# Kernel optimization log

Measured on AMD Instinct MI355X. Metric: run time of the kernel, lower is better.

The kernel has to match this reference:

```python
import jax, jax.numpy as jnp
import numpy as np

B, S, HQ, HKV, D = 2, 2048, 32, 8, 128
ROPE_BASE = 10000.0
NEG_INF = -1e9


def setup_inputs() -> dict:
    key = jax.random.key(0)
    kq, kk, kv = jax.random.split(key, 3)
    q = jax.random.normal(kq, (B, S, HQ, D), dtype=jnp.float32)
    k = jax.random.normal(kk, (B, S, HKV, D), dtype=jnp.float32)
    v = jax.random.normal(kv, (B, S, HKV, D), dtype=jnp.float32)
    # Llama rotary tables: [S, D] with freqs duplicated across the two halves
    inv_freq = 1.0 / (ROPE_BASE ** (jnp.arange(0, D, 2, dtype=jnp.float32) / D))
    freqs = jnp.arange(S, dtype=jnp.float32)[:, None] * inv_freq[None, :]  # [S, D/2]
    emb = jnp.concatenate([freqs, freqs], axis=-1)  # [S, D]
    cos = jnp.cos(emb)
    sin = jnp.sin(emb)
    # causal additive mask [B, 1, S, S]: 0 on/below diagonal, -1e9 above
    causal = jnp.tril(jnp.ones((S, S), dtype=bool))
    attention_mask = jnp.where(causal, 0.0, NEG_INF).astype(jnp.float32)
    attention_mask = jnp.broadcast_to(attention_mask[None, None], (B, 1, S, S))
    return {
        "query_states": q,
        "key_states": k,
        "value_states": v,
        "cos": cos,
        "sin": sin,
        "attention_mask": attention_mask,
        "softmax_scale": float(1.0 / np.sqrt(D)),
    }


def _rotate_half(x):
    h = x.shape[-1] // 2
    return jnp.concatenate([-x[..., h:], x[..., :h]], axis=-1)


def _apply_rope(x, cos, sin):
    # x: [B, S, H, D]; cos/sin: [S, D] -> broadcast over batch and heads
    c = cos[None, :, None, :]
    s = sin[None, :, None, :]
    return x * c + _rotate_half(x) * s


def reference(query_states, key_states, value_states, cos, sin, attention_mask, softmax_scale):
    if attention_mask.ndim == 4 and attention_mask.shape[1] == 1:
        attention_mask = attention_mask[:, 0]  # [B, S, S]
    q = _apply_rope(query_states, cos, sin)          # [B, S, HQ, D]
    k = _apply_rope(key_states, cos, sin)            # [B, S, HKV, D]
    v = value_states                                  # [B, S, HKV, D]
    groups = q.shape[2] // k.shape[2]
    k = jnp.repeat(k, groups, axis=2)                 # [B, S, HQ, D]
    v = jnp.repeat(v, groups, axis=2)
    scores = jnp.einsum("bqhd,bkhd->bhqk", q, k) * softmax_scale
    scores = scores + attention_mask[:, None, :, :]   # broadcast over heads
    probs = jax.nn.softmax(scores, axis=-1)
    out = jnp.einsum("bhqk,bkhd->bqhd", probs, v)     # [B, S, HQ, D]
    return out
```

## Files before the change

kernel.cpp:

```cpp
#include <hip/hip_runtime.h>
#include <stdint.h>

typedef unsigned short u16;
typedef unsigned int   u32;
typedef short bf16x8 __attribute__((ext_vector_type(8)));
typedef u16   u16x8  __attribute__((ext_vector_type(8)));
typedef u16   u16x4  __attribute__((ext_vector_type(4)));
typedef float f32x4  __attribute__((ext_vector_type(4)));

#define B_   2
#define S_   2048
#define HQ_  32
#define HKV_ 8
#define D_   128
#define SC2  0.1275174457530659f

#define KR_ELEMS (B_*HKV_*S_*D_)

#define KT_BLOCKS ((B_*S_*HKV_*16) / 256)
#define VT_BLOCKS (B_*HKV_*(S_/64))

#define SWZ(x) ((x) ^ (((x) >> 3) & 0x70))

__device__ __forceinline__ float b2f(u16 x) { return __uint_as_float(((u32)x) << 16); }
__device__ __forceinline__ u16 f2b(float f) {
  u32 u = __float_as_uint(f);
  return (u16)((u + 0x7FFFu + ((u >> 16) & 1u)) >> 16);
}
__device__ __forceinline__ bool is_f32(const void* cs) {
  return ((const u32*)cs)[0] == 0x3F800000u;
}

#if __has_builtin(__builtin_amdgcn_exp2f)
#define EXP2(x) __builtin_amdgcn_exp2f(x)
#else
#define EXP2(x) exp2f(x)
#endif

__device__ __forceinline__ void pl32(u32& a, u32& b) {
  auto r = __builtin_amdgcn_permlane32_swap((int)a, (int)b, false, false);
  a = (u32)r[0]; b = (u32)r[1];
}
__device__ __forceinline__ void pl16(u32& a, u32& b) {
  auto r = __builtin_amdgcn_permlane16_swap((int)a, (int)b, false, false);
  a = (u32)r[0]; b = (u32)r[1];
}
__device__ __forceinline__ float qredmax(float x) {
  u32 a = __float_as_uint(x), b = a;
  pl16(a, b);
  float m = fmaxf(__uint_as_float(a), __uint_as_float(b));
  u32 c = __float_as_uint(m), d = c;
  pl32(c, d);
  return fmaxf(__uint_as_float(c), __uint_as_float(d));
}
__device__ __forceinline__ float qredsum(float x) {
  u32 a = __float_as_uint(x), b = a;
  pl16(a, b);
  float m = __uint_as_float(a) + __uint_as_float(b);
  u32 c = __float_as_uint(m), d = c;
  pl32(c, d);
  return __uint_as_float(c) + __uint_as_float(d);
}
__device__ __forceinline__ u32 cvtpk(float lo, float hi) {
  u32 r;
  asm("v_cvt_pk_bf16_f32 %0, %1, %2" : "=v"(r) : "v"(lo), "v"(hi));
  return r;
}

__device__ __forceinline__ void gload16(const u16* g, u16* l) {
  __builtin_amdgcn_global_load_lds(
      (const __attribute__((address_space(1))) u32*)g,
      (__attribute__((address_space(3))) u32*)l, 16, 0, 0);
}

__global__ __launch_bounds__(256) void rope_pre(
    const void* __restrict__ kin, const void* __restrict__ vin,
    const void* __restrict__ cs, const void* __restrict__ sn, u16* __restrict__ ws)
{
  const bool f32 = is_f32(cs);
  const int bx = blockIdx.x;
  const int t  = threadIdx.x;
  __shared__ u16 tile[64 * 136];

  if (bx < KT_BLOCKS) {
    int tid = bx*256 + t;
    int j4 = tid & 15;
    int s  = (tid >> 4) & (S_ - 1);
    int h  = (tid >> 15) & (HKV_ - 1);
    int b  = tid >> 18;
    int gi = ((b*S_ + s)*HKV_ + h)*D_ + 4*j4;
    int ci = s*D_ + 4*j4;
    float xa[4], xb[4], c[4], si[4];
    if (f32) {
      const float* kf = (const float*)kin;
      f32x4 a0 = *(const f32x4*)(kf + gi);
      f32x4 b0 = *(const f32x4*)(kf + gi + 64);
      f32x4 c0 = *(const f32x4*)((const float*)cs + ci);
      f32x4 s0 = *(const f32x4*)((const float*)sn + ci);
#pragma unroll
      for (int e = 0; e < 4; ++e) { xa[e]=a0[e]; xb[e]=b0[e]; c[e]=c0[e]; si[e]=s0[e]; }
    } else {
      const u16* kb16 = (const u16*)kin;
      u16x4 a0 = *(const u16x4*)(kb16 + gi);
      u16x4 b0 = *(const u16x4*)(kb16 + gi + 64);
      u16x4 c0 = *(const u16x4*)((const u16*)cs + ci);
      u16x4 s0 = *(const u16x4*)((const u16*)sn + ci);
#pragma unroll
      for (int e = 0; e < 4; ++e) { xa[e]=b2f(a0[e]); xb[e]=b2f(b0[e]); c[e]=b2f(c0[e]); si[e]=b2f(s0[e]); }
    }
    u16 o0[4], o1[4];
#pragma unroll
    for (int e = 0; e < 4; ++e) {
      o0[e] = f2b(xa[e]*c[e] - xb[e]*si[e]);
      o1[e] = f2b(xb[e]*c[e] + xa[e]*si[e]);
    }
    int oi = ((b*HKV_ + h)*S_ + s)*D_ + 4*j4;
    *(u16x4*)(ws + oi)      = *(u16x4*)o0;
    *(u16x4*)(ws + oi + 64) = *(u16x4*)o1;
  } else {
    int vb = bx - KT_BLOCKS;
    int sb = vb & 31;
    int h  = (vb >> 5) & (HKV_ - 1);
    int b  = vb >> 8;
    int s0 = sb * 64;
#pragma unroll
    for (int it = 0; it < 8; ++it) {
      int task = it*256 + t;
      int c4 = task & 31;
      int r  = task >> 5;
      int gi = ((b*S_ + s0 + r)*HKV_ + h)*D_ + 4*c4;
      u16 e[4];
      if (f32) {
        f32x4 a = *(const f32x4*)((const float*)vin + gi);
#pragma unroll
        for (int j = 0; j < 4; ++j) e[j] = f2b(a[j]);
      } else {
        u16x4 a = *(const u16x4*)((const u16*)vin + gi);
#pragma unroll
        for (int j = 0; j < 4; ++j) e[j] = a[j];
      }
      *(u16x4*)&tile[r*136 + 4*c4] = *(u16x4*)e;
    }
    __syncthreads();
    u32* vtd = (u32*)(ws + KR_ELEMS) + (b*HKV_ + h)*D_*(S_/2);
#pragma unroll
    for (int it = 0; it < 16; ++it) {
      int task = it*256 + t;
      int sp = task & 31, d = task >> 5;
      u32 lo = tile[(2*sp)*136 + d];
      u32 hi = tile[(2*sp + 1)*136 + d];
      vtd[d*(S_/2) + s0/2 + sp] = lo | (hi << 16);
    }
  }
}

__global__ __launch_bounds__(256, 3) void flash_attn(
    const void* __restrict__ qg, const void* __restrict__ cs, const void* __restrict__ sn,
    const u16* __restrict__ ws, float* __restrict__ out)
{
  __shared__ __attribute__((aligned(16))) u16 lds[16384];
  char* ldsc = (char*)lds;

  const bool f32 = is_f32(cs);
  const int t = threadIdx.x;
  const int lane = t & 63, w = t >> 6;
  const int lq = lane & 15, quad = lane >> 4;

  const int kq = (lq*64 + quad*16) ^ (((lq >> 1) & 7) << 4);

  int bx = blockIdx.x;
  int g = bx & 7, ii = bx >> 3;
  int combo = g*2 + (ii >> 6);
  int b = combo >> 3, kvh = combo & 7;
  int rr = ii & 63;
  int h   = kvh*4 + (rr & 3);
  int qt  = 15 - (rr >> 2);
  int q0  = qt * 128;
  const int nkb  = 4*qt + 4;
  const int diag = 4*qt + w;

  const u16* Kr = ws + (b*HKV_ + kvh)*S_*D_;
  const u16* Vt = ws + KR_ELEMS + (b*HKV_ + kvh)*D_*S_;

  const int aK0 = t*16, aK1 = t*16 + 4096;
  const int lA0 = SWZ(aK0), lA1 = SWZ(aK1);
  const u16* kg0 = Kr + ((lA0 >> 6) & 31)*D_ + (lA0 >> 11)*32 + ((lA0 >> 4) & 3)*8;
  const u16* kg1 = Kr + ((lA1 >> 6) & 31)*D_ + (lA1 >> 11)*32 + ((lA1 >> 4) & 3)*8;
  const u16* vg0 = Vt + (lA0 >> 6)*S_ + ((lA0 >> 4) & 3)*8;
  const u16* vg1 = Vt + (lA1 >> 6)*S_ + ((lA1 >> 4) & 3)*8;

#define STAGE(bufbyte, n0v) do {                                   \
    gload16(kg0 + (n0v)*D_, (u16*)(ldsc + (bufbyte) + aK0));       \
    gload16(kg1 + (n0v)*D_, (u16*)(ldsc + (bufbyte) + aK1));       \
    gload16(vg0 + (n0v),    (u16*)(ldsc + (bufbyte) + 8192 + aK0));\
    gload16(vg1 + (n0v),    (u16*)(ldsc + (bufbyte) + 8192 + aK1));\
  } while (0)

#pragma unroll
  for (int it = 0; it < 4; ++it) {
    int tp = it*256 + t;
    int row = tp >> 3, j = tp & 7;
    int qbase = ((b*S_ + q0 + row)*HQ_ + h)*D_ + 8*j;
    int cbase = (q0 + row)*D_ + 8*j;
    float a[8], bb[8], cc[8], ssv[8];
    if (f32) {
      const float* qf32 = (const float*)qg;
      f32x4 a0 = *(const f32x4*)(qf32 + qbase);
      f32x4 a1 = *(const f32x4*)(qf32 + qbase + 4);
      f32x4 b0 = *(const f32x4*)(qf32 + qbase + 64);
      f32x4 b1 = *(const f32x4*)(qf32 + qbase + 68);
      f32x4 c0 = *(const f32x4*)((const float*)cs + cbase);
      f32x4 c1 = *(const f32x4*)((const float*)cs + cbase + 4);
      f32x4 s0 = *(const f32x4*)((const float*)sn + cbase);
      f32x4 s1 = *(const f32x4*)((const float*)sn + cbase + 4);
#pragma unroll
      for (int e = 0; e < 4; ++e) {
        a[e] = a0[e];  a[4+e] = a1[e];  bb[e] = b0[e]; bb[4+e] = b1[e];
        cc[e] = c0[e]; cc[4+e] = c1[e]; ssv[e] = s0[e]; ssv[4+e] = s1[e];
      }
    } else {
      const u16* qb16 = (const u16*)qg;
      u16x8 xa = *(const u16x8*)(qb16 + qbase);
      u16x8 xb = *(const u16x8*)(qb16 + qbase + 64);
      u16x8 cv = *(const u16x8*)((const u16*)cs + cbase);
      u16x8 sv = *(const u16x8*)((const u16*)sn + cbase);
#pragma unroll
      for (int e = 0; e < 8; ++e) {
        a[e] = b2f(xa[e]); bb[e] = b2f(xb[e]);
        cc[e] = b2f(cv[e]); ssv[e] = b2f(sv[e]);
      }
    }
    u16 o0[8], o1[8];
#pragma unroll
    for (int e = 0; e < 8; ++e) {
      float C2 = cc[e]*SC2, S2 = ssv[e]*SC2;
      o0[e] = f2b(a[e]*C2 - bb[e]*S2);
      o1[e] = f2b(bb[e]*C2 + a[e]*S2);
    }
    int A0 = (j >> 2)*8192 + row*64 + (j & 3)*16;
    int A1 = A0 + 16384;
    *(u16x8*)(ldsc + SWZ(A0)) = *(u16x8*)o0;
    *(u16x8*)(ldsc + SWZ(A1)) = *(u16x8*)o1;
  }
  __syncthreads();
  bf16x8 qfA[4], qfB[4];
#pragma unroll
  for (int c = 0; c < 4; ++c) {
    qfA[c] = *(const bf16x8*)(ldsc + c*8192 + w*2048 + kq);
    qfB[c] = *(const bf16x8*)(ldsc + c*8192 + w*2048 + 1024 + kq);
  }
  asm volatile("s_waitcnt lgkmcnt(0)" ::: "memory");
  __syncthreads();

  f32x4 oA[8], oB[8];
#pragma unroll
  for (int dt = 0; dt < 8; ++dt) { oA[dt] = (f32x4){0,0,0,0}; oB[dt] = (f32x4){0,0,0,0}; }
  float mA = -1e30f, lA = 0.f, mB = -1e30f, lB = 0.f;
  const int qrowA = q0 + 32*w + lq;

  STAGE(0, 0);

  for (int kb = 0; kb < nkb; ++kb) {
    const int cur = kb & 1;
    asm volatile("" ::: "memory");
    __builtin_amdgcn_s_barrier();
    asm volatile("" ::: "memory");
    if (kb + 1 < nkb) {
      STAGE((cur ^ 1) << 14, (kb + 1)*32);
      asm volatile("s_waitcnt vmcnt(4)" ::: "memory");
    } else {
      asm volatile("s_waitcnt vmcnt(0)" ::: "memory");
    }
    __builtin_amdgcn_s_barrier();
    asm volatile("" ::: "memory");

    if (kb > diag) continue;

    const char* tb = ldsc + (cur << 14) + kq;

    f32x4 sA0 = {0,0,0,0}, sA1 = {0,0,0,0}, sB0 = {0,0,0,0}, sB1 = {0,0,0,0};
#pragma unroll
    for (int c = 0; c < 4; ++c) {
      bf16x8 k0 = *(const bf16x8*)(tb + c*2048);
      bf16x8 k1 = *(const bf16x8*)(tb + c*2048 + 1024);
      sA0 = __builtin_amdgcn_mfma_f32_16x16x32_bf16(k0, qfA[c], sA0, 0, 0, 0);
      sA1 = __builtin_amdgcn_mfma_f32_16x16x32_bf16(k1, qfA[c], sA1, 0, 0, 0);
      sB0 = __builtin_amdgcn_mfma_f32_16x16x32_bf16(k0, qfB[c], sB0, 0, 0, 0);
      sB1 = __builtin_amdgcn_mfma_f32_16x16x32_bf16(k1, qfB[c], sB1, 0, 0, 0);
    }

    float a0[4], a1[4], b0[4], b1[4];
#pragma unroll
    for (int r = 0; r < 4; ++r) { a0[r]=sA0[r]; a1[r]=sA1[r]; b0[r]=sB0[r]; b1[r]=sB1[r]; }
    if (kb == diag) {
#pragma unroll
      for (int r = 0; r < 4; ++r) {
        bool over = (quad*4 + r > lq);
        if (over) a0[r] = -1e30f;
        a1[r] = -1e30f;
        if (over) b1[r] = -1e30f;
      }
    }

    float mxA = fmaxf(fmaxf(fmaxf(a0[0],a0[1]), fmaxf(a0[2],a0[3])),
                      fmaxf(fmaxf(a1[0],a1[1]), fmaxf(a1[2],a1[3])));
    float mxB = fmaxf(fmaxf(fmaxf(b0[0],b0[1]), fmaxf(b0[2],b0[3])),
                      fmaxf(fmaxf(b1[0],b1[1]), fmaxf(b1[2],b1[3])));
    mxA = qredmax(mxA);
    mxB = qredmax(mxB);
    if (!__all((mxA - mA <= 11.5f) && (mxB - mB <= 11.5f))) {
      float mnA = fmaxf(mA, mxA), alA = EXP2(mA - mnA);
      float mnB = fmaxf(mB, mxB), alB = EXP2(mB - mnB);
      lA *= alA; lB *= alB;
#pragma unroll
      for (int dt = 0; dt < 8; ++dt) {
#pragma unroll
        for (int r = 0; r < 4; ++r) { oA[dt][r] *= alA; oB[dt][r] *= alB; }
      }
      mA = mnA; mB = mnB;
    }
    float pA0[4], pA1[4], pB0[4], pB1[4];
    float rsA = 0.f, rsB = 0.f;
#pragma unroll
    for (int r = 0; r < 4; ++r) {
      pA0[r] = EXP2(a0[r] - mA); pA1[r] = EXP2(a1[r] - mA);
      pB0[r] = EXP2(b0[r] - mB); pB1[r] = EXP2(b1[r] - mB);
      rsA += pA0[r] + pA1[r];    rsB += pB0[r] + pB1[r];
    }
    lA += qredsum(rsA);
    lB += qredsum(rsB);

    u32 YA0 = cvtpk(pA0[0], pA0[1]), YA1 = cvtpk(pA0[2], pA0[3]);
    u32 ZA0 = cvtpk(pA1[0], pA1[1]), ZA1 = cvtpk(pA1[2], pA1[3]);
    pl32(YA0, ZA0); pl16(YA0, ZA0);
    pl32(YA1, ZA1); pl16(YA1, ZA1);
    u32 YB0 = cvtpk(pB0[0], pB0[1]), YB1 = cvtpk(pB0[2], pB0[3]);
    u32 ZB0 = cvtpk(pB1[0], pB1[1]), ZB1 = cvtpk(pB1[2], pB1[3]);
    pl32(YB0, ZB0); pl16(YB0, ZB0);
    pl32(YB1, ZB1); pl16(YB1, ZB1);
    union { u32 wd[4]; bf16x8 v; } puA, puB;
    puA.wd[0] = YA0; puA.wd[1] = YA1; puA.wd[2] = ZA0; puA.wd[3] = ZA1;
    puB.wd[0] = YB0; puB.wd[1] = YB1; puB.wd[2] = ZB0; puB.wd[3] = ZB1;
    bf16x8 pfA = puA.v, pfB = puB.v;

#pragma unroll
    for (int dt = 0; dt < 8; ++dt) {
      bf16x8 vf = *(const bf16x8*)(tb + 8192 + dt*1024);
      oA[dt] = __builtin_amdgcn_mfma_f32_16x16x32_bf16(vf, pfA, oA[dt], 0, 0, 0);
      oB[dt] = __builtin_amdgcn_mfma_f32_16x16x32_bf16(vf, pfB, oB[dt], 0, 0, 0);
    }
  }

  float invA = 1.0f / lA, invB = 1.0f / lB;
  float* opA = out + ((b*S_ + qrowA)*HQ_ + h)*D_ + quad*4;
  float* opB = opA + 16*HQ_*D_;
#pragma unroll
  for (int dt = 0; dt < 8; ++dt) {
    f32x4 va = { oA[dt][0]*invA, oA[dt][1]*invA, oA[dt][2]*invA, oA[dt][3]*invA };
    f32x4 vb = { oB[dt][0]*invB, oB[dt][1]*invB, oB[dt][2]*invB, oB[dt][3]*invB };
    *(f32x4*)(opA + dt*16) = va;
    *(f32x4*)(opB + dt*16) = vb;
  }
#undef STAGE
}

extern "C" void kernel_launch(void* const* d_in, const int* in_sizes, int n_in,
                              void* d_out, int out_size, void* d_ws, size_t ws_size,
                              hipStream_t stream) {
  const void* q  = d_in[0];
  const void* k  = d_in[1];
  const void* v  = d_in[2];
  const void* cs = d_in[3];
  const void* sn = d_in[4];
  u16*   ws  = (u16*)d_ws;
  float* out = (float*)d_out;

  rope_pre<<<KT_BLOCKS + VT_BLOCKS, 256, 0, stream>>>(k, v, cs, sn, ws);
  flash_attn<<<B_*HQ_*(S_/128), 256, 0, stream>>>(q, cs, sn, ws, out);
}
```

Baseline: 264.3 us.

## Pair complementary causal q-tiles per block and double the K/V tile to 64 keys

Each block now handles two query tiles (qt and 15-qt), which balances causal work across 512 blocks instead of launching 1024 blocks of uneven length. The K/V stage grows to 64 keys per step with a 64KB double buffer, so occupancy drops to 2 blocks per CU, and s_setprio is placed around the MFMA sections. The pipeline now waits for each prefetch to finish at the end of the iteration with a single barrier, in place of the earlier partial vmcnt wait. This trades occupancy for fewer barriers and less per-tile overhead.

```diff
diff --git a/kernel.cpp b/kernel.cpp
--- a/kernel.cpp
+++ b/kernel.cpp
@@ -65,6 +65,15 @@
   u32 r;
   asm("v_cvt_pk_bf16_f32 %0, %1, %2" : "=v"(r) : "v"(lo), "v"(hi));
   return r;
+}
+__device__ __forceinline__ bf16x8 pack_pt(const float* p0, const float* p1) {
+  u32 Y0 = cvtpk(p0[0], p0[1]), Y1 = cvtpk(p0[2], p0[3]);
+  u32 Z0 = cvtpk(p1[0], p1[1]), Z1 = cvtpk(p1[2], p1[3]);
+  pl32(Y0, Z0); pl16(Y0, Z0);
+  pl32(Y1, Z1); pl16(Y1, Z1);
+  union { u32 wd[4]; bf16x8 v; } pu;
+  pu.wd[0] = Y0; pu.wd[1] = Y1; pu.wd[2] = Z0; pu.wd[3] = Z1;
+  return pu.v;
 }
 
 __device__ __forceinline__ void gload16(const u16* g, u16* l) {
@@ -154,11 +163,11 @@
   }
 }
 
-__global__ __launch_bounds__(256, 3) void flash_attn(
+__global__ __launch_bounds__(256, 2) void flash_attn(
     const void* __restrict__ qg, const void* __restrict__ cs, const void* __restrict__ sn,
     const u16* __restrict__ ws, float* __restrict__ out)
 {
-  __shared__ __attribute__((aligned(16))) u16 lds[16384];
+  __shared__ __attribute__((aligned(16))) u16 lds[32768];
   char* ldsc = (char*)lds;
 
   const bool f32 = is_f32(cs);
@@ -170,196 +179,227 @@
 
   int bx = blockIdx.x;
   int g = bx & 7, ii = bx >> 3;
-  int combo = g*2 + (ii >> 6);
+  int combo = g*2 + (ii >> 5);
   int b = combo >> 3, kvh = combo & 7;
-  int rr = ii & 63;
+  int rr = ii & 31;
   int h   = kvh*4 + (rr & 3);
-  int qt  = 15 - (rr >> 2);
-  int q0  = qt * 128;
-  const int nkb  = 4*qt + 4;
-  const int diag = 4*qt + w;
+  int qtp = rr >> 2;
 
   const u16* Kr = ws + (b*HKV_ + kvh)*S_*D_;
   const u16* Vt = ws + KR_ELEMS + (b*HKV_ + kvh)*D_*S_;
 
-  const int aK0 = t*16, aK1 = t*16 + 4096;
-  const int lA0 = SWZ(aK0), lA1 = SWZ(aK1);
-  const u16* kg0 = Kr + ((lA0 >> 6) & 31)*D_ + (lA0 >> 11)*32 + ((lA0 >> 4) & 3)*8;
-  const u16* kg1 = Kr + ((lA1 >> 6) & 31)*D_ + (lA1 >> 11)*32 + ((lA1 >> 4) & 3)*8;
-  const u16* vg0 = Vt + (lA0 >> 6)*S_ + ((lA0 >> 4) & 3)*8;
-  const u16* vg1 = Vt + (lA1 >> 6)*S_ + ((lA1 >> 4) & 3)*8;
-
-#define STAGE(bufbyte, n0v) do {                                   \
-    gload16(kg0 + (n0v)*D_, (u16*)(ldsc + (bufbyte) + aK0));       \
-    gload16(kg1 + (n0v)*D_, (u16*)(ldsc + (bufbyte) + aK1));       \
-    gload16(vg0 + (n0v),    (u16*)(ldsc + (bufbyte) + 8192 + aK0));\
-    gload16(vg1 + (n0v),    (u16*)(ldsc + (bufbyte) + 8192 + aK1));\
+  const int base = t*16;
+  const u16* kgp[4];
+  const u16* vgp[4];
+#pragma unroll
+  for (int i = 0; i < 4; ++i) {
+    int a = base + i*4096;
+    int l = SWZ(a);
+    int kkt = l >> 13, kc = (l >> 11) & 3, kkey = (l >> 6) & 31, ke = (l >> 4) & 3;
+    kgp[i] = Kr + (kkt*32 + kkey)*D_ + kc*32 + ke*8;
+    int vkt = l >> 13, vd = (l >> 6) & 127, vk = (l >> 4) & 3;
+    vgp[i] = Vt + vd*S_ + vkt*32 + vk*8;
+  }
+
+#define STAGE(bufbyte, n0v) do {                                            \
+    _Pragma("unroll")                                                       \
+    for (int i_ = 0; i_ < 4; ++i_) {                                        \
+      gload16(kgp[i_] + (n0v)*D_,                                           \
+              (u16*)(ldsc + (bufbyte) + base + i_*4096));                   \
+      gload16(vgp[i_] + (n0v),                                              \
+              (u16*)(ldsc + (bufbyte) + 16384 + base + i_*4096));           \
+    }                                                                       \
   } while (0)
 
-#pragma unroll
-  for (int it = 0; it < 4; ++it) {
-    int tp = it*256 + t;
-    int row = tp >> 3, j = tp & 7;
-    int qbase = ((b*S_ + q0 + row)*HQ_ + h)*D_ + 8*j;
-    int cbase = (q0 + row)*D_ + 8*j;
-    float a[8], bb[8], cc[8], ssv[8];
-    if (f32) {
-      const float* qf32 = (const float*)qg;
-      f32x4 a0 = *(const f32x4*)(qf32 + qbase);
-      f32x4 a1 = *(const f32x4*)(qf32 + qbase + 4);
-      f32x4 b0 = *(const f32x4*)(qf32 + qbase + 64);
-      f32x4 b1 = *(const f32x4*)(qf32 + qbase + 68);
-      f32x4 c0 = *(const f32x4*)((const float*)cs + cbase);
-      f32x4 c1 = *(const f32x4*)((const float*)cs + cbase + 4);
-      f32x4 s0 = *(const f32x4*)((const float*)sn + cbase);
-      f32x4 s1 = *(const f32x4*)((const float*)sn + cbase + 4);
-#pragma unroll
-      for (int e = 0; e < 4; ++e) {
-        a[e] = a0[e];  a[4+e] = a1[e];  bb[e] = b0[e]; bb[4+e] = b1[e];
-        cc[e] = c0[e]; cc[4+e] = c1[e]; ssv[e] = s0[e]; ssv[4+e] = s1[e];
+  for (int half = 0; half < 2; ++half) {
+    int qt = half ? (15 - qtp) : qtp;
+    int q0 = qt * 128;
+    if (half) __syncthreads();
+
+#pragma unroll
+    for (int it = 0; it < 4; ++it) {
+      int tp = it*256 + t;
+      int row = tp >> 3, j = tp & 7;
+      int qbase = ((b*S_ + q0 + row)*HQ_ + h)*D_ + 8*j;
+      int cbase = (q0 + row)*D_ + 8*j;
+      float a[8], bb[8], cc[8], ssv[8];
+      if (f32) {
+        const float* qf32 = (const float*)qg;
+        f32x4 a0 = *(const f32x4*)(qf32 + qbase);
+        f32x4 a1 = *(const f32x4*)(qf32 + qbase + 4);
+        f32x4 b0 = *(const f32x4*)(qf32 + qbase + 64);
+        f32x4 b1 = *(const f32x4*)(qf32 + qbase + 68);
+        f32x4 c0 = *(const f32x4*)((const float*)cs + cbase);
+        f32x4 c1 = *(const f32x4*)((const float*)cs + cbase + 4);
+        f32x4 s0 = *(const f32x4*)((const float*)sn + cbase);
+        f32x4 s1 = *(const f32x4*)((const float*)sn + cbase + 4);
+#pragma unroll
+        for (int e = 0; e < 4; ++e) {
+          a[e] = a0[e];  a[4+e] = a1[e];  bb[e] = b0[e]; bb[4+e] = b1[e];
+          cc[e] = c0[e]; cc[4+e] = c1[e]; ssv[e] = s0[e]; ssv[4+e] = s1[e];
+        }
+      } else {
+        const u16* qb16 = (const u16*)qg;
+        u16x8 xa = *(const u16x8*)(qb16 + qbase);
+        u16x8 xb = *(const u16x8*)(qb16 + qbase + 64);
+        u16x8 cv = *(const u16x8*)((const u16*)cs + cbase);
+        u16x8 sv = *(const u16x8*)((const u16*)sn + cbase);
+#pragma unroll
+        for (int e = 0; e < 8; ++e) {
+          a[e] = b2f(xa[e]); bb[e] = b2f(xb[e]);
+          cc[e] = b2f(cv[e]); ssv[e] = b2f(sv[e]);
+        }
       }
-    } else {
-      const u16* qb16 = (const u16*)qg;
-      u16x8 xa = *(const u16x8*)(qb16 + qbase);
-      u16x8 xb = *(const u16x8*)(qb16 + qbase + 64);
-      u16x8 cv = *(const u16x8*)((const u16*)cs + cbase);
-      u16x8 sv = *(const u16x8*)((const u16*)sn + cbase);
+      u16 o0[8], o1[8];
 #pragma unroll
       for (int e = 0; e < 8; ++e) {
-        a[e] = b2f(xa[e]); bb[e] = b2f(xb[e]);
-        cc[e] = b2f(cv[e]); ssv[e] = b2f(sv[e]);
+        float C2 = cc[e]*SC2, S2 = ssv[e]*SC2;
+        o0[e] = f2b(a[e]*C2 - bb[e]*S2);
+        o1[e] = f2b(bb[e]*C2 + a[e]*S2);
       }
-    }
-    u16 o0[8], o1[8];
-#pragma unroll
-    for (int e = 0; e < 8; ++e) {
-      float C2 = cc[e]*SC2, S2 = ssv[e]*SC2;
-      o0[e] = f2b(a[e]*C2 - bb[e]*S2);
-      o1[e] = f2b(bb[e]*C2 + a[e]*S2);
-    }
-    int A0 = (j >> 2)*8192 + row*64 + (j & 3)*16;
-    int A1 = A0 + 16384;
-    *(u16x8*)(ldsc + SWZ(A0)) = *(u16x8*)o0;
-    *(u16x8*)(ldsc + SWZ(A1)) = *(u16x8*)o1;
-  }
-  __syncthreads();
-  bf16x8 qfA[4], qfB[4];
-#pragma unroll
-  for (int c = 0; c < 4; ++c) {
-    qfA[c] = *(const bf16x8*)(ldsc + c*8192 + w*2048 + kq);
-    qfB[c] = *(const bf16x8*)(ldsc + c*8192 + w*2048 + 1024 + kq);
-  }
-  asm volatile("s_waitcnt lgkmcnt(0)" ::: "memory");
-  __syncthreads();
-
-  f32x4 oA[8], oB[8];
-#pragma unroll
-  for (int dt = 0; dt < 8; ++dt) { oA[dt] = (f32x4){0,0,0,0}; oB[dt] = (f32x4){0,0,0,0}; }
-  float mA = -1e30f, lA = 0.f, mB = -1e30f, lB = 0.f;
-  const int qrowA = q0 + 32*w + lq;
-
-  STAGE(0, 0);
-
-  for (int kb = 0; kb < nkb; ++kb) {
-    const int cur = kb & 1;
-    asm volatile("" ::: "memory");
+      int A0 = (j >> 2)*8192 + row*64 + (j & 3)*16;
+      int A1 = A0 + 16384;
+      *(u16x8*)(ldsc + SWZ(A0)) = *(u16x8*)o0;
+      *(u16x8*)(ldsc + SWZ(A1)) = *(u16x8*)o1;
+    }
+    __syncthreads();
+    bf16x8 qfA[4], qfB[4];
+#pragma unroll
+    for (int c = 0; c < 4; ++c) {
+      qfA[c] = *(const bf16x8*)(ldsc + c*8192 + w*2048 + kq);
+      qfB[c] = *(const bf16x8*)(ldsc + c*8192 + w*2048 + 1024 + kq);
+    }
+    asm volatile("s_waitcnt lgkmcnt(0)" ::: "memory");
+    __syncthreads();
+
+    f32x4 oA[8], oB[8];
+#pragma unroll
+    for (int dt = 0; dt < 8; ++dt) { oA[dt] = (f32x4){0,0,0,0}; oB[dt] = (f32x4){0,0,0,0}; }
+    float mA = -1e30f, lA = 0.f, mB = -1e30f, lB = 0.f;
+    const int qrowA = q0 + 32*w + lq;
+    const int nkb = 2*qt + 2;
+    const int kbD = 2*qt + (w >> 1);
+
+    STAGE(0, 0);
+    asm volatile("s_waitcnt vmcnt(0)" ::: "memory");
     __builtin_amdgcn_s_barrier();
     asm volatile("" ::: "memory");
-    if (kb + 1 < nkb) {
-      STAGE((cur ^ 1) << 14, (kb + 1)*32);
-      asm volatile("s_waitcnt vmcnt(4)" ::: "memory");
-    } else {
-      asm volatile("s_waitcnt vmcnt(0)" ::: "memory");
-    }
-    __builtin_amdgcn_s_barrier();
-    asm volatile("" ::: "memory");
-
-    if (kb > diag) continue;
-
-    const char* tb = ldsc + (cur << 14) + kq;
-
-    f32x4 sA0 = {0,0,0,0}, sA1 = {0,0,0,0}, sB0 = {0,0,0,0}, sB1 = {0,0,0,0};
-#pragma unroll
-    for (int c = 0; c < 4; ++c) {
-      bf16x8 k0 = *(const bf16x8*)(tb + c*2048);
-      bf16x8 k1 = *(const bf16x8*)(tb + c*2048 + 1024);
-      sA0 = __builtin_amdgcn_mfma_f32_16x16x32_bf16(k0, qfA[c], sA0, 0, 0, 0);
-      sA1 = __builtin_amdgcn_mfma_f32_16x16x32_bf16(k1, qfA[c], sA1, 0, 0, 0);
-      sB0 = __builtin_amdgcn_mfma_f32_16x16x32_bf16(k0, qfB[c], sB0, 0, 0, 0);
-      sB1 = __builtin_amdgcn_mfma_f32_16x16x32_bf16(k1, qfB[c], sB1, 0, 0, 0);
-    }
-
-    float a0[4], a1[4], b0[4], b1[4];
-#pragma unroll
-    for (int r = 0; r < 4; ++r) { a0[r]=sA0[r]; a1[r]=sA1[r]; b0[r]=sB0[r]; b1[r]=sB1[r]; }
-    if (kb == diag) {
-#pragma unroll
-      for (int r = 0; r < 4; ++r) {
-        bool over = (quad*4 + r > lq);
-        if (over) a0[r] = -1e30f;
-        a1[r] = -1e30f;
-        if (over) b1[r] = -1e30f;
+
+    int cur = 0;
+    for (int kb = 0; kb < nkb; ++kb) {
+      if (kb + 1 < nkb) STAGE((cur ^ 1) << 15, (kb + 1)*64);
+      asm volatile("" ::: "memory");
+
+      if (kb <= kbD) {
+        const int n0 = kb * 64;
+        const char* tbk = ldsc + (cur << 15) + kq;
+        const char* tbv = tbk + 16384;
+
+        f32x4 sA[2][2], sB[2][2];
+#pragma unroll
+        for (int kt = 0; kt < 2; ++kt)
+#pragma unroll
+          for (int st = 0; st < 2; ++st) { sA[kt][st] = (f32x4){0,0,0,0}; sB[kt][st] = (f32x4){0,0,0,0}; }
+        __builtin_amdgcn_s_setprio(1);
+#pragma unroll
+        for (int c = 0; c < 4; ++c) {
+#pragma unroll
+          for (int kt = 0; kt < 2; ++kt) {
+            bf16x8 k0 = *(const bf16x8*)(tbk + kt*8192 + c*2048);
+            bf16x8 k1 = *(const bf16x8*)(tbk + kt*8192 + c*2048 + 1024);
+            sA[kt][0] = __builtin_amdgcn_mfma_f32_16x16x32_bf16(k0, qfA[c], sA[kt][0], 0, 0, 0);
+            sA[kt][1] = __builtin_amdgcn_mfma_f32_16x16x32_bf16(k1, qfA[c], sA[kt][1], 0, 0, 0);
+            sB[kt][0] = __builtin_amdgcn_mfma_f32_16x16x32_bf16(k0, qfB[c], sB[kt][0], 0, 0, 0);
+            sB[kt][1] = __builtin_amdgcn_mfma_f32_16x16x32_bf16(k1, qfB[c], sB[kt][1], 0, 0, 0);
+          }
+        }
+        __builtin_amdgcn_s_setprio(0);
+
+        if (kb == kbD) {
+#pragma unroll
+          for (int kt = 0; kt < 2; ++kt)
+#pragma unroll
+            for (int st = 0; st < 2; ++st)
+#pragma unroll
+              for (int r = 0; r < 4; ++r) {
+                int key = n0 + kt*32 + st*16 + quad*4 + r;
+                if (key > qrowA)      sA[kt][st][r] = -1e30f;
+                if (key > qrowA + 16) sB[kt][st][r] = -1e30f;
+              }
+        }
+
+        float mxA = -1e30f, mxB = -1e30f;
+#pragma unroll
+        for (int kt = 0; kt < 2; ++kt)
+#pragma unroll
+          for (int st = 0; st < 2; ++st)
+#pragma unroll
+            for (int r = 0; r < 4; ++r) {
+              mxA = fmaxf(mxA, sA[kt][st][r]);
+              mxB = fmaxf(mxB, sB[kt][st][r]);
+            }
+        mxA = qredmax(mxA);
+        mxB = qredmax(mxB);
+        if (!__all((mxA - mA <= 11.5f) && (mxB - mB <= 11.5f))) {
+          float mnA = fmaxf(mA, mxA), alA = EXP2(mA - mnA);
+          float mnB = fmaxf(mB, mxB), alB = EXP2(mB - mnB);
+          lA *= alA; lB *= alB;
+#pragma unroll
+          for (int dt = 0; dt < 8; ++dt)
+#pragma unroll
+            for (int r = 0; r < 4; ++r) { oA[dt][r] *= alA; oB[dt][r] *= alB; }
+          mA = mnA; mB = mnB;
+        }
+        float pA[2][2][4], pB[2][2][4];
+        float rsA = 0.f, rsB = 0.f;
+#pragma unroll
+        for (int kt = 0; kt < 2; ++kt)
+#pragma unroll
+          for (int st = 0; st < 2; ++st)
+#pragma unroll
+            for (int r = 0; r < 4; ++r) {
+              pA[kt][st][r] = EXP2(sA[kt][st][r] - mA);
+              pB[kt][st][r] = EXP2(sB[kt][st][r] - mB);
+              rsA += pA[kt][st][r];
+              rsB += pB[kt][st][r];
+            }
+        lA += qredsum(rsA);
+        lB += qredsum(rsB);
+
+        bf16x8 pfA0 = pack_pt(pA[0][0], pA[0][1]);
+        bf16x8 pfA1 = pack_pt(pA[1][0], pA[1][1]);
+        bf16x8 pfB0 = pack_pt(pB[0][0], pB[0][1]);
+        bf16x8 pfB1 = pack_pt(pB[1][0], pB[1][1]);
+
+        __builtin_amdgcn_s_setprio(1);
+#pragma unroll
+        for (int dt = 0; dt < 8; ++dt) {
+          bf16x8 v0 = *(const bf16x8*)(tbv + dt*1024);
+          bf16x8 v1 = *(const bf16x8*)(tbv + 8192 + dt*1024);
+          oA[dt] = __builtin_amdgcn_mfma_f32_16x16x32_bf16(v0, pfA0, oA[dt], 0, 0, 0);
+          oB[dt] = __builtin_amdgcn_mfma_f32_16x16x32_bf16(v0, pfB0, oB[dt], 0, 0, 0);
+          oA[dt] = __builtin_amdgcn_mfma_f32_16x16x32_bf16(v1, pfA1, oA[dt], 0, 0, 0);
+          oB[dt] = __builtin_amdgcn_mfma_f32_16x16x32_bf16(v1, pfB1, oB[dt], 0, 0, 0);
+        }
+        __builtin_amdgcn_s_setprio(0);
       }
-    }
-
-    float mxA = fmaxf(fmaxf(fmaxf(a0[0],a0[1]), fmaxf(a0[2],a0[3])),
-                      fmaxf(fmaxf(a1[0],a1[1]), fmaxf(a1[2],a1[3])));
-    float mxB = fmaxf(fmaxf(fmaxf(b0[0],b0[1]), fmaxf(b0[2],b0[3])),
-                      fmaxf(fmaxf(b1[0],b1[1]), fmaxf(b1[2],b1[3])));
-    mxA = qredmax(mxA);
-    mxB = qredmax(mxB);
-    if (!__all((mxA - mA <= 11.5f) && (mxB - mB <= 11.5f))) {
-      float mnA = fmaxf(mA, mxA), alA = EXP2(mA - mnA);
-      float mnB = fmaxf(mB, mxB), alB = EXP2(mB - mnB);
-      lA *= alA; lB *= alB;
-#pragma unroll
-      for (int dt = 0; dt < 8; ++dt) {
-#pragma unroll
-        for (int r = 0; r < 4; ++r) { oA[dt][r] *= alA; oB[dt][r] *= alB; }
-      }
-      mA = mnA; mB = mnB;
-    }
-    float pA0[4], pA1[4], pB0[4], pB1[4];
-    float rsA = 0.f, rsB = 0.f;
-#pragma unroll
-    for (int r = 0; r < 4; ++r) {
-      pA0[r] = EXP2(a0[r] - mA); pA1[r] = EXP2(a1[r] - mA);
-      pB0[r] = EXP2(b0[r] - mB); pB1[r] = EXP2(b1[r] - mB);
-      rsA += pA0[r] + pA1[r];    rsB += pB0[r] + pB1[r];
-    }
-    lA += qredsum(rsA);
-    lB += qredsum(rsB);
-
-    u32 YA0 = cvtpk(pA0[0], pA0[1]), YA1 = cvtpk(pA0[2], pA0[3]);
-    u32 ZA0 = cvtpk(pA1[0], pA1[1]), ZA1 = cvtpk(pA1[2], pA1[3]);
-    pl32(YA0, ZA0); pl16(YA0, ZA0);
-    pl32(YA1, ZA1); pl16(YA1, ZA1);
-    u32 YB0 = cvtpk(pB0[0], pB0[1]), YB1 = cvtpk(pB0[2], pB0[3]);
-    u32 ZB0 = cvtpk(pB1[0], pB1[1]), ZB1 = cvtpk(pB1[2], pB1[3]);
-    pl32(YB0, ZB0); pl16(YB0, ZB0);
-    pl32(YB1, ZB1); pl16(YB1, ZB1);
-    union { u32 wd[4]; bf16x8 v; } puA, puB;
-    puA.wd[0] = YA0; puA.wd[1] = YA1; puA.wd[2] = ZA0; puA.wd[3] = ZA1;
-    puB.wd[0] = YB0; puB.wd[1] = YB1; puB.wd[2] = ZB0; puB.wd[3] = ZB1;
-    bf16x8 pfA = puA.v, pfB = puB.v;
-
+
+      asm volatile("s_waitcnt vmcnt(0) lgkmcnt(0)" ::: "memory");
+      __builtin_amdgcn_s_barrier();
+      asm volatile("" ::: "memory");
+      cur ^= 1;
+    }
+
+    float invA = 1.0f / lA, invB = 1.0f / lB;
+    float* opA = out + ((b*S_ + qrowA)*HQ_ + h)*D_ + quad*4;
+    float* opB = opA + 16*HQ_*D_;
 #pragma unroll
     for (int dt = 0; dt < 8; ++dt) {
-      bf16x8 vf = *(const bf16x8*)(tb + 8192 + dt*1024);
-      oA[dt] = __builtin_amdgcn_mfma_f32_16x16x32_bf16(vf, pfA, oA[dt], 0, 0, 0);
-      oB[dt] = __builtin_amdgcn_mfma_f32_16x16x32_bf16(vf, pfB, oB[dt], 0, 0, 0);
-    }
-  }
-
-  float invA = 1.0f / lA, invB = 1.0f / lB;
-  float* opA = out + ((b*S_ + qrowA)*HQ_ + h)*D_ + quad*4;
-  float* opB = opA + 16*HQ_*D_;
-#pragma unroll
-  for (int dt = 0; dt < 8; ++dt) {
-    f32x4 va = { oA[dt][0]*invA, oA[dt][1]*invA, oA[dt][2]*invA, oA[dt][3]*invA };
-    f32x4 vb = { oB[dt][0]*invB, oB[dt][1]*invB, oB[dt][2]*invB, oB[dt][3]*invB };
-    *(f32x4*)(opA + dt*16) = va;
-    *(f32x4*)(opB + dt*16) = vb;
+      f32x4 va = { oA[dt][0]*invA, oA[dt][1]*invA, oA[dt][2]*invA, oA[dt][3]*invA };
+      f32x4 vb = { oB[dt][0]*invB, oB[dt][1]*invB, oB[dt][2]*invB, oB[dt][3]*invB };
+      *(f32x4*)(opA + dt*16) = va;
+      *(f32x4*)(opB + dt*16) = vb;
+    }
   }
 #undef STAGE
 }
@@ -376,5 +416,5 @@
   float* out = (float*)d_out;
 
   rope_pre<<<KT_BLOCKS + VT_BLOCKS, 256, 0, stream>>>(k, v, cs, sn, ws);
-  flash_attn<<<B_*HQ_*(S_/128), 256, 0, stream>>>(q, cs, sn, ws, out);
-}
+  flash_attn<<<512, 256, 0, stream>>>(q, cs, sn, ws, out);
+}
```

Measured after the change: 243.7 us. 1.08x faster.

## Pair short and long causal query tiles per block, reshape K/V pipeline loop

Applied to the files above, without the earlier changes.

Each workgroup now processes two query tiles, qt and 15-qt, one after the other, so every block does the same amount of causal work. The grid is halved to 512 blocks. The K/V double-buffer loop is restructured so the next tile's prefetch is issued before compute, with one wait and barrier at the end of each iteration. The change also raises launch-bounds occupancy to 4 and wraps the MFMA sections in s_setprio. The goal is to remove tail imbalance from causal work skew and barrier overhead, at the cost of more register pressure and serialising the two tiles inside a block.

```diff
diff --git a/kernel.cpp b/kernel.cpp
--- a/kernel.cpp
+++ b/kernel.cpp
@@ -65,6 +65,15 @@
   u32 r;
   asm("v_cvt_pk_bf16_f32 %0, %1, %2" : "=v"(r) : "v"(lo), "v"(hi));
   return r;
+}
+__device__ __forceinline__ bf16x8 pack_pt(const float* p0, const float* p1) {
+  u32 Y0 = cvtpk(p0[0], p0[1]), Y1 = cvtpk(p0[2], p0[3]);
+  u32 Z0 = cvtpk(p1[0], p1[1]), Z1 = cvtpk(p1[2], p1[3]);
+  pl32(Y0, Z0); pl16(Y0, Z0);
+  pl32(Y1, Z1); pl16(Y1, Z1);
+  union { u32 wd[4]; bf16x8 v; } pu;
+  pu.wd[0] = Y0; pu.wd[1] = Y1; pu.wd[2] = Z0; pu.wd[3] = Z1;
+  return pu.v;
 }
 
 __device__ __forceinline__ void gload16(const u16* g, u16* l) {
@@ -154,7 +163,7 @@
   }
 }
 
-__global__ __launch_bounds__(256, 3) void flash_attn(
+__global__ __launch_bounds__(256, 4) void flash_attn(
     const void* __restrict__ qg, const void* __restrict__ cs, const void* __restrict__ sn,
     const u16* __restrict__ ws, float* __restrict__ out)
 {
@@ -170,14 +179,11 @@
 
   int bx = blockIdx.x;
   int g = bx & 7, ii = bx >> 3;
-  int combo = g*2 + (ii >> 6);
+  int combo = g*2 + (ii >> 5);
   int b = combo >> 3, kvh = combo & 7;
-  int rr = ii & 63;
+  int rr = ii & 31;
   int h   = kvh*4 + (rr & 3);
-  int qt  = 15 - (rr >> 2);
-  int q0  = qt * 128;
-  const int nkb  = 4*qt + 4;
-  const int diag = 4*qt + w;
+  int qtp = rr >> 2;
 
   const u16* Kr = ws + (b*HKV_ + kvh)*S_*D_;
   const u16* Vt = ws + KR_ELEMS + (b*HKV_ + kvh)*D_*S_;
@@ -196,170 +202,169 @@
     gload16(vg1 + (n0v),    (u16*)(ldsc + (bufbyte) + 8192 + aK1));\
   } while (0)
 
-#pragma unroll
-  for (int it = 0; it < 4; ++it) {
-    int tp = it*256 + t;
-    int row = tp >> 3, j = tp & 7;
-    int qbase = ((b*S_ + q0 + row)*HQ_ + h)*D_ + 8*j;
-    int cbase = (q0 + row)*D_ + 8*j;
-    float a[8], bb[8], cc[8], ssv[8];
-    if (f32) {
-      const float* qf32 = (const float*)qg;
-      f32x4 a0 = *(const f32x4*)(qf32 + qbase);
-      f32x4 a1 = *(const f32x4*)(qf32 + qbase + 4);
-      f32x4 b0 = *(const f32x4*)(qf32 + qbase + 64);
-      f32x4 b1 = *(const f32x4*)(qf32 + qbase + 68);
-      f32x4 c0 = *(const f32x4*)((const float*)cs + cbase);
-      f32x4 c1 = *(const f32x4*)((const float*)cs + cbase + 4);
-      f32x4 s0 = *(const f32x4*)((const float*)sn + cbase);
-      f32x4 s1 = *(const f32x4*)((const float*)sn + cbase + 4);
-#pragma unroll
-      for (int e = 0; e < 4; ++e) {
-        a[e] = a0[e];  a[4+e] = a1[e];  bb[e] = b0[e]; bb[4+e] = b1[e];
-        cc[e] = c0[e]; cc[4+e] = c1[e]; ssv[e] = s0[e]; ssv[4+e] = s1[e];
+  for (int half = 0; half < 2; ++half) {
+    int qt = half ? (15 - qtp) : qtp;
+    int q0 = qt * 128;
+    if (half) __syncthreads();
+
+#pragma unroll
+    for (int it = 0; it < 4; ++it) {
+      int tp = it*256 + t;
+      int row = tp >> 3, j = tp & 7;
+      int qbase = ((b*S_ + q0 + row)*HQ_ + h)*D_ + 8*j;
+      int cbase = (q0 + row)*D_ + 8*j;
+      float a[8], bb[8], cc[8], ssv[8];
+      if (f32) {
+        const float* qf32 = (const float*)qg;
+        f32x4 a0 = *(const f32x4*)(qf32 + qbase);
+        f32x4 a1 = *(const f32x4*)(qf32 + qbase + 4);
+        f32x4 b0 = *(const f32x4*)(qf32 + qbase + 64);
+        f32x4 b1 = *(const f32x4*)(qf32 + qbase + 68);
+        f32x4 c0 = *(const f32x4*)((const float*)cs + cbase);
+        f32x4 c1 = *(const f32x4*)((const float*)cs + cbase + 4);
+        f32x4 s0 = *(const f32x4*)((const float*)sn + cbase);
+        f32x4 s1 = *(const f32x4*)((const float*)sn + cbase + 4);
+#pragma unroll
+        for (int e = 0; e < 4; ++e) {
+          a[e] = a0[e];  a[4+e] = a1[e];  bb[e] = b0[e]; bb[4+e] = b1[e];
+          cc[e] = c0[e]; cc[4+e] = c1[e]; ssv[e] = s0[e]; ssv[4+e] = s1[e];
+        }
+      } else {
+        const u16* qb16 = (const u16*)qg;
+        u16x8 xa = *(const u16x8*)(qb16 + qbase);
+        u16x8 xb = *(const u16x8*)(qb16 + qbase + 64);
+        u16x8 cv = *(const u16x8*)((const u16*)cs + cbase);
+        u16x8 sv = *(const u16x8*)((const u16*)sn + cbase);
+#pragma unroll
+        for (int e = 0; e < 8; ++e) {
+          a[e] = b2f(xa[e]); bb[e] = b2f(xb[e]);
+          cc[e] = b2f(cv[e]); ssv[e] = b2f(sv[e]);
+        }
       }
-    } else {
-      const u16* qb16 = (const u16*)qg;
-      u16x8 xa = *(const u16x8*)(qb16 + qbase);
-      u16x8 xb = *(const u16x8*)(qb16 + qbase + 64);
-      u16x8 cv = *(const u16x8*)((const u16*)cs + cbase);
-      u16x8 sv = *(const u16x8*)((const u16*)sn + cbase);
+      u16 o0[8], o1[8];
 #pragma unroll
       for (int e = 0; e < 8; ++e) {
-        a[e] = b2f(xa[e]); bb[e] = b2f(xb[e]);
-        cc[e] = b2f(cv[e]); ssv[e] = b2f(sv[e]);
+        float C2 = cc[e]*SC2, S2 = ssv[e]*SC2;
+        o0[e] = f2b(a[e]*C2 - bb[e]*S2);
+        o1[e] = f2b(bb[e]*C2 + a[e]*S2);
       }
-    }
-    u16 o0[8], o1[8];
-#pragma unroll
-    for (int e = 0; e < 8; ++e) {
-      float C2 = cc[e]*SC2, S2 = ssv[e]*SC2;
-      o0[e] = f2b(a[e]*C2 - bb[e]*S2);
-      o1[e] = f2b(bb[e]*C2 + a[e]*S2);
-    }
-    int A0 = (j >> 2)*8192 + row*64 + (j & 3)*16;
-    int A1 = A0 + 16384;
-    *(u16x8*)(ldsc + SWZ(A0)) = *(u16x8*)o0;
-    *(u16x8*)(ldsc + SWZ(A1)) = *(u16x8*)o1;
-  }
-  __syncthreads();
-  bf16x8 qfA[4], qfB[4];
-#pragma unroll
-  for (int c = 0; c < 4; ++c) {
-    qfA[c] = *(const bf16x8*)(ldsc + c*8192 + w*2048 + kq);
-    qfB[c] = *(const bf16x8*)(ldsc + c*8192 + w*2048 + 1024 + kq);
-  }
-  asm volatile("s_waitcnt lgkmcnt(0)" ::: "memory");
-  __syncthreads();
-
-  f32x4 oA[8], oB[8];
-#pragma unroll
-  for (int dt = 0; dt < 8; ++dt) { oA[dt] = (f32x4){0,0,0,0}; oB[dt] = (f32x4){0,0,0,0}; }
-  float mA = -1e30f, lA = 0.f, mB = -1e30f, lB = 0.f;
-  const int qrowA = q0 + 32*w + lq;
-
-  STAGE(0, 0);
-
-  for (int kb = 0; kb < nkb; ++kb) {
-    const int cur = kb & 1;
-    asm volatile("" ::: "memory");
+      int A0 = (j >> 2)*8192 + row*64 + (j & 3)*16;
+      int A1 = A0 + 16384;
+      *(u16x8*)(ldsc + SWZ(A0)) = *(u16x8*)o0;
+      *(u16x8*)(ldsc + SWZ(A1)) = *(u16x8*)o1;
+    }
+    __syncthreads();
+    bf16x8 qfA[4], qfB[4];
+#pragma unroll
+    for (int c = 0; c < 4; ++c) {
+      qfA[c] = *(const bf16x8*)(ldsc + c*8192 + w*2048 + kq);
+      qfB[c] = *(const bf16x8*)(ldsc + c*8192 + w*2048 + 1024 + kq);
+    }
+    asm volatile("s_waitcnt lgkmcnt(0)" ::: "memory");
+    __syncthreads();
+
+    f32x4 oA[8], oB[8];
+#pragma unroll
+    for (int dt = 0; dt < 8; ++dt) { oA[dt] = (f32x4){0,0,0,0}; oB[dt] = (f32x4){0,0,0,0}; }
+    float mA = -1e30f, lA = 0.f, mB = -1e30f, lB = 0.f;
+    const int qrowA = q0 + 32*w + lq;
+    const int nkb = 4*qt + 4;
+    const int kbD = 4*qt + w;
+
+    STAGE(0, 0);
+    asm volatile("s_waitcnt vmcnt(0)" ::: "memory");
     __builtin_amdgcn_s_barrier();
     asm volatile("" ::: "memory");
-    if (kb + 1 < nkb) {
-      STAGE((cur ^ 1) << 14, (kb + 1)*32);
-      asm volatile("s_waitcnt vmcnt(4)" ::: "memory");
-    } else {
-      asm volatile("s_waitcnt vmcnt(0)" ::: "memory");
-    }
-    __builtin_amdgcn_s_barrier();
-    asm volatile("" ::: "memory");
-
-    if (kb > diag) continue;
-
-    const char* tb = ldsc + (cur << 14) + kq;
-
-    f32x4 sA0 = {0,0,0,0}, sA1 = {0,0,0,0}, sB0 = {0,0,0,0}, sB1 = {0,0,0,0};
-#pragma unroll
-    for (int c = 0; c < 4; ++c) {
-      bf16x8 k0 = *(const bf16x8*)(tb + c*2048);
-      bf16x8 k1 = *(const bf16x8*)(tb + c*2048 + 1024);
-      sA0 = __builtin_amdgcn_mfma_f32_16x16x32_bf16(k0, qfA[c], sA0, 0, 0, 0);
-      sA1 = __builtin_amdgcn_mfma_f32_16x16x32_bf16(k1, qfA[c], sA1, 0, 0, 0);
-      sB0 = __builtin_amdgcn_mfma_f32_16x16x32_bf16(k0, qfB[c], sB0, 0, 0, 0);
-      sB1 = __builtin_amdgcn_mfma_f32_16x16x32_bf16(k1, qfB[c], sB1, 0, 0, 0);
-    }
-
-    float a0[4], a1[4], b0[4], b1[4];
-#pragma unroll
-    for (int r = 0; r < 4; ++r) { a0[r]=sA0[r]; a1[r]=sA1[r]; b0[r]=sB0[r]; b1[r]=sB1[r]; }
-    if (kb == diag) {
-#pragma unroll
-      for (int r = 0; r < 4; ++r) {
-        bool over = (quad*4 + r > lq);
-        if (over) a0[r] = -1e30f;
-        a1[r] = -1e30f;
-        if (over) b1[r] = -1e30f;
+
+    int cur = 0;
+    for (int kb = 0; kb < nkb; ++kb) {
+      if (kb + 1 < nkb) STAGE((cur ^ 1) << 14, (kb + 1)*32);
+      asm volatile("" ::: "memory");
+
+      if (kb <= kbD) {
+        const char* tbk = ldsc + (cur << 14) + kq;
+        const char* tbv = tbk + 8192;
+
+        f32x4 sA0 = {0,0,0,0}, sA1 = {0,0,0,0};
+        f32x4 sB0 = {0,0,0,0}, sB1 = {0,0,0,0};
+        __builtin_amdgcn_s_setprio(1);
+#pragma unroll
+        for (int c = 0; c < 4; ++c) {
+          bf16x8 k0 = *(const bf16x8*)(tbk + c*2048);
+          bf16x8 k1 = *(const bf16x8*)(tbk + c*2048 + 1024);
+          sA0 = __builtin_amdgcn_mfma_f32_16x16x32_bf16(k0, qfA[c], sA0, 0, 0, 0);
+          sA1 = __builtin_amdgcn_mfma_f32_16x16x32_bf16(k1, qfA[c], sA1, 0, 0, 0);
+          sB0 = __builtin_amdgcn_mfma_f32_16x16x32_bf16(k0, qfB[c], sB0, 0, 0, 0);
+          sB1 = __builtin_amdgcn_mfma_f32_16x16x32_bf16(k1, qfB[c], sB1, 0, 0, 0);
+        }
+        __builtin_amdgcn_s_setprio(0);
+
+        if (kb == kbD) {
+#pragma unroll
+          for (int r = 0; r < 4; ++r) {
+            bool over = (quad*4 + r > lq);
+            if (over) sA0[r] = -1e30f;
+            sA1[r] = -1e30f;
+            if (over) sB1[r] = -1e30f;
+          }
+        }
+
+        float mxA = fmaxf(fmaxf(fmaxf(sA0[0], sA0[1]), fmaxf(sA0[2], sA0[3])),
+                          fmaxf(fmaxf(sA1[0], sA1[1]), fmaxf(sA1[2], sA1[3])));
+        float mxB = fmaxf(fmaxf(fmaxf(sB0[0], sB0[1]), fmaxf(sB0[2], sB0[3])),
+                          fmaxf(fmaxf(sB1[0], sB1[1]), fmaxf(sB1[2], sB1[3])));
+        mxA = qredmax(mxA);
+        mxB = qredmax(mxB);
+        if (!__all((mxA - mA <= 11.5f) && (mxB - mB <= 11.5f))) {
+          float mnA = fmaxf(mA, mxA), alA = EXP2(mA - mnA);
+          float mnB = fmaxf(mB, mxB), alB = EXP2(mB - mnB);
+          lA *= alA; lB *= alB;
+#pragma unroll
+          for (int dt = 0; dt < 8; ++dt)
+#pragma unroll
+            for (int r = 0; r < 4; ++r) { oA[dt][r] *= alA; oB[dt][r] *= alB; }
+          mA = mnA; mB = mnB;
+        }
+        float pA0[4], pA1[4], pB0[4], pB1[4];
+        float rsA = 0.f, rsB = 0.f;
+#pragma unroll
+        for (int r = 0; r < 4; ++r) {
+          pA0[r] = EXP2(sA0[r] - mA); pA1[r] = EXP2(sA1[r] - mA);
+          pB0[r] = EXP2(sB0[r] - mB); pB1[r] = EXP2(sB1[r] - mB);
+          rsA += pA0[r] + pA1[r];     rsB += pB0[r] + pB1[r];
+        }
+        lA += qredsum(rsA);
+        lB += qredsum(rsB);
+
+        bf16x8 pfA = pack_pt(pA0, pA1);
+        bf16x8 pfB = pack_pt(pB0, pB1);
+
+        __builtin_amdgcn_s_setprio(1);
+#pragma unroll
+        for (int dt = 0; dt < 8; ++dt) {
+          bf16x8 vf = *(const bf16x8*)(tbv + dt*1024);
+          oA[dt] = __builtin_amdgcn_mfma_f32_16x16x32_bf16(vf, pfA, oA[dt], 0, 0, 0);
+          oB[dt] = __builtin_amdgcn_mfma_f32_16x16x32_bf16(vf, pfB, oB[dt], 0, 0, 0);
+        }
+        __builtin_amdgcn_s_setprio(0);
       }
-    }
-
-    float mxA = fmaxf(fmaxf(fmaxf(a0[0],a0[1]), fmaxf(a0[2],a0[3])),
-                      fmaxf(fmaxf(a1[0],a1[1]), fmaxf(a1[2],a1[3])));
-    float mxB = fmaxf(fmaxf(fmaxf(b0[0],b0[1]), fmaxf(b0[2],b0[3])),
-                      fmaxf(fmaxf(b1[0],b1[1]), fmaxf(b1[2],b1[3])));
-    mxA = qredmax(mxA);
-    mxB = qredmax(mxB);
-    if (!__all((mxA - mA <= 11.5f) && (mxB - mB <= 11.5f))) {
-      float mnA = fmaxf(mA, mxA), alA = EXP2(mA - mnA);
-      float mnB = fmaxf(mB, mxB), alB = EXP2(mB - mnB);
-      lA *= alA; lB *= alB;
-#pragma unroll
-      for (int dt = 0; dt < 8; ++dt) {
-#pragma unroll
-        for (int r = 0; r < 4; ++r) { oA[dt][r] *= alA; oB[dt][r] *= alB; }
-      }
-      mA = mnA; mB = mnB;
-    }
-    float pA0[4], pA1[4], pB0[4], pB1[4];
-    float rsA = 0.f, rsB = 0.f;
-#pragma unroll
-    for (int r = 0; r < 4; ++r) {
-      pA0[r] = EXP2(a0[r] - mA); pA1[r] = EXP2(a1[r] - mA);
-      pB0[r] = EXP2(b0[r] - mB); pB1[r] = EXP2(b1[r] - mB);
-      rsA += pA0[r] + pA1[r];    rsB += pB0[r] + pB1[r];
-    }
-    lA += qredsum(rsA);
-    lB += qredsum(rsB);
-
-    u32 YA0 = cvtpk(pA0[0], pA0[1]), YA1 = cvtpk(pA0[2], pA0[3]);
-    u32 ZA0 = cvtpk(pA1[0], pA1[1]), ZA1 = cvtpk(pA1[2], pA1[3]);
-    pl32(YA0, ZA0); pl16(YA0, ZA0);
-    pl32(YA1, ZA1); pl16(YA1, ZA1);
-    u32 YB0 = cvtpk(pB0[0], pB0[1]), YB1 = cvtpk(pB0[2], pB0[3]);
-    u32 ZB0 = cvtpk(pB1[0], pB1[1]), ZB1 = cvtpk(pB1[2], pB1[3]);
-    pl32(YB0, ZB0); pl16(YB0, ZB0);
-    pl32(YB1, ZB1); pl16(YB1, ZB1);
-    union { u32 wd[4]; bf16x8 v; } puA, puB;
-    puA.wd[0] = YA0; puA.wd[1] = YA1; puA.wd[2] = ZA0; puA.wd[3] = ZA1;
-    puB.wd[0] = YB0; puB.wd[1] = YB1; puB.wd[2] = ZB0; puB.wd[3] = ZB1;
-    bf16x8 pfA = puA.v, pfB = puB.v;
-
+
+      asm volatile("s_waitcnt vmcnt(0) lgkmcnt(0)" ::: "memory");
+      __builtin_amdgcn_s_barrier();
+      asm volatile("" ::: "memory");
+      cur ^= 1;
+    }
+
+    float invA = 1.0f / lA, invB = 1.0f / lB;
+    float* opA = out + ((b*S_ + qrowA)*HQ_ + h)*D_ + quad*4;
+    float* opB = opA + 16*HQ_*D_;
 #pragma unroll
     for (int dt = 0; dt < 8; ++dt) {
-      bf16x8 vf = *(const bf16x8*)(tb + 8192 + dt*1024);
-      oA[dt] = __builtin_amdgcn_mfma_f32_16x16x32_bf16(vf, pfA, oA[dt], 0, 0, 0);
-      oB[dt] = __builtin_amdgcn_mfma_f32_16x16x32_bf16(vf, pfB, oB[dt], 0, 0, 0);
-    }
-  }
-
-  float invA = 1.0f / lA, invB = 1.0f / lB;
-  float* opA = out + ((b*S_ + qrowA)*HQ_ + h)*D_ + quad*4;
-  float* opB = opA + 16*HQ_*D_;
-#pragma unroll
-  for (int dt = 0; dt < 8; ++dt) {
-    f32x4 va = { oA[dt][0]*invA, oA[dt][1]*invA, oA[dt][2]*invA, oA[dt][3]*invA };
-    f32x4 vb = { oB[dt][0]*invB, oB[dt][1]*invB, oB[dt][2]*invB, oB[dt][3]*invB };
-    *(f32x4*)(opA + dt*16) = va;
-    *(f32x4*)(opB + dt*16) = vb;
+      f32x4 va = { oA[dt][0]*invA, oA[dt][1]*invA, oA[dt][2]*invA, oA[dt][3]*invA };
+      f32x4 vb = { oB[dt][0]*invB, oB[dt][1]*invB, oB[dt][2]*invB, oB[dt][3]*invB };
+      *(f32x4*)(opA + dt*16) = va;
+      *(f32x4*)(opB + dt*16) = vb;
+    }
   }
 #undef STAGE
 }
@@ -376,5 +381,5 @@
   float* out = (float*)d_out;
 
   rope_pre<<<KT_BLOCKS + VT_BLOCKS, 256, 0, stream>>>(k, v, cs, sn, ws);
-  flash_attn<<<B_*HQ_*(S_/128), 256, 0, stream>>>(q, cs, sn, ws, out);
-}
+  flash_attn<<<512, 256, 0, stream>>>(q, cs, sn, ws, out);
+}
```

After: 343.4 us. 1.3x slower.
